# Performance work log

Hardware: AMD Instinct MI355X
Metric: run time of the kernel (lower is better)

## Reference

```python
import jax, jax.numpy as jnp
import numpy as np

VOCAB, EMB, HID, OUT = 50257, 256, 512, 2

def setup_inputs() -> dict:
    key = jax.random.key(0)
    ks = jax.random.split(key, 8)
    s_e = 1.0  # nn.Embedding default N(0,1)
    emb = jax.random.normal(ks[0], (VOCAB, EMB), dtype=jnp.float32) * s_e
    emb = emb.at[0].set(0.0)  # padding_idx=0
    def lin(k1, k2, fan_in, fan_out):
        bound = 1.0 / np.sqrt(fan_in)
        w = jax.random.uniform(k1, (fan_out, fan_in), minval=-bound, maxval=bound, dtype=jnp.float32)
        b = jax.random.uniform(k2, (fan_out,), minval=-bound, maxval=bound, dtype=jnp.float32)
        return w, b
    Ww, Wb = lin(ks[1], ks[2], EMB, HID)
    Uw, Ub = lin(ks[3], ks[4], HID, HID)
    Vw, Vb = lin(ks[5], ks[6], HID, OUT)
    x = jax.random.randint(ks[7], (128, 512), 0, VOCAB, dtype=jnp.int64)
    return {"x": x, "emb": emb, "Ww": Ww, "Wb": Wb, "Uw": Uw, "Ub": Ub, "Vw": Vw, "Vb": Vb}

def reference(x, emb, Ww, Wb, Uw, Ub, Vw, Vb):
    # x: [B, T] int tokens -> embed: [B, T, E]
    xe = emb[x]
    # Precompute input projections for all timesteps in one big GEMM: [B, T, H]
    wx = jnp.einsum('bte,he->bth', xe, Ww) + Wb
    B = x.shape[0]
    h0 = jnp.zeros((B, Uw.shape[0]), dtype=xe.dtype)
    def step(h, wx_t):
        h_new = jnp.tanh(wx_t + h @ Uw.T + Ub)
        return h_new, None
    hT, _ = jax.lax.scan(step, h0, jnp.swapaxes(wx, 0, 1))  # scan over time [T, B, H]
    logits = hT @ Vw.T + Vb  # [B, OUT]
    return logits
```

## Files before the change

kernel.cpp:

```cpp
#include <hip/hip_runtime.h>
#include <hip/hip_bf16.h>
#include <math.h>


#define VOCAB   50257
#define T_STEPS 512
#define HID     512
#define EMB     256

typedef __bf16 bf16x8 __attribute__((ext_vector_type(8)));
typedef float  f32x4  __attribute__((ext_vector_type(4)));
typedef float  f32x2  __attribute__((ext_vector_type(2)));
typedef int    i32x4  __attribute__((ext_vector_type(4)));

__device__ inline float ldf(const void* p, long i, bool f32) {
    if (f32) return ((const float*)p)[i];
    unsigned bits = ((unsigned)((const unsigned short*)p)[i]) << 16;
    return __uint_as_float(bits);
}
__device__ inline void stf(void* p, long i, float v, bool f32) {
    if (f32) { ((float*)p)[i] = v; return; }
    unsigned b = __float_as_uint(v);
    unsigned r = (b + 0x7fffu + ((b >> 16) & 1u)) >> 16;
    ((unsigned short*)p)[i] = (unsigned short)r;
}
__device__ inline unsigned short f2bf(float v) {
    unsigned b = __float_as_uint(v);
    return (unsigned short)((b + 0x7fffu + ((b >> 16) & 1u)) >> 16);
}
__device__ inline float bf2f(unsigned short u) {
    return __uint_as_float(((unsigned)u) << 16);
}
__device__ inline int get_tok(const int* x, int idx, bool x64) {
    unsigned u = (unsigned)(x64 ? x[2 * idx] : x[idx]);
    return (u < (unsigned)VOCAB) ? (int)u : 0;
}
__device__ inline int detect_flags(const int* x, const void* emb) {
    int allz = 1;
    const unsigned short* e16 = (const unsigned short*)emb;
    for (int i = 256; i < 320; ++i) allz &= (e16[i] == 0);
    int x64 = 1;
    for (int j = 1; j < 16; j += 2) x64 &= (x[j] == 0);
    return allz | (x64 << 1);
}
__device__ inline float tanh_f(float x) {
    float ax = fabsf(x);
    float e  = __expf(-2.0f * ax);
    float t  = (1.0f - e) * __builtin_amdgcn_rcpf(1.0f + e);
    return copysignf(t, x);
}
__device__ inline unsigned tq(float v) {
    float x = fminf(3.5f, fmaxf(-3.5f, v));
    float s = x * x;
    float num = x * fmaf(s, fmaf(s, 127.0f, 13335.0f), 120015.0f);
    float den = fmaf(s, fmaf(s, 15.0f, 420.0f), 945.0f);
    float f = fmaf(num, __builtin_amdgcn_rcpf(den), 12582912.0f);
    return __float_as_uint(f) & 0xffu;
}
__device__ inline unsigned tq2(float a, float b) {
    f32x2 x;
    x.x = fminf(3.5f, fmaxf(-3.5f, a));
    x.y = fminf(3.5f, fmaxf(-3.5f, b));
    f32x2 s   = x * x;
    f32x2 num = x * (s * (s * 127.0f + 13335.0f) + 120015.0f);
    f32x2 den = s * (s * 15.0f + 420.0f) + 945.0f;
    float f0 = fmaf(num.x, __builtin_amdgcn_rcpf(den.x), 12582912.0f);
    float f1 = fmaf(num.y, __builtin_amdgcn_rcpf(den.y), 12582912.0f);
    return (__float_as_uint(f0) & 0xffu) | ((__float_as_uint(f1) & 0xffu) << 8);
}

#define XEPAD 264
__global__ __launch_bounds__(1024) void wx_gemm(
    const int* __restrict__ x, const void* __restrict__ embv,
    const void* __restrict__ Wwv, const void* __restrict__ Wbv,
    const void* __restrict__ Ubv, unsigned char* __restrict__ ws)
{
    __shared__ __align__(16) __hip_bfloat16 xe_s[64][XEPAD];
    __shared__ int flags_s;
    const int t = blockIdx.x, tid = threadIdx.x;
    if (tid == 0) flags_s = detect_flags(x, embv);
    __syncthreads();
    const bool f32w = (flags_s & 1) != 0;
    const bool x64  = (flags_s & 2) != 0;

    const int w = tid >> 6, lane = tid & 63, ln = lane & 15, q = lane >> 4;

    bf16x8 bf[2][8];
    float  bias[2];
#pragma unroll
    for (int tn = 0; tn < 2; ++tn) {
        long n = w * 32 + tn * 16 + ln;
        bias[tn] = ldf(Wbv, n, f32w) + ldf(Ubv, n, f32w);
#pragma unroll
        for (int kt = 0; kt < 8; ++kt) {
            bf16x8 v;
#pragma unroll
            for (int j = 0; j < 8; ++j)
                v[j] = (__bf16)ldf(Wwv, n * EMB + kt * 32 + q * 8 + j, f32w);
            bf[tn][kt] = v;
        }
    }

    for (int half = 0; half < 2; ++half) {
        {
            int row = tid >> 4, sub = tid & 15;
            int tok = get_tok(x, (half * 64 + row) * T_STEPS + t, x64);
#pragma unroll
            for (int i = 0; i < 4; ++i) {
                int col = sub * 4 + i * 64;
                float v0, v1, v2, v3;
                if (f32w) {
                    const float4 vv = *(const float4*)((const float*)embv
                                        + (long)tok * EMB + col);
                    v0 = vv.x; v1 = vv.y; v2 = vv.z; v3 = vv.w;
                } else {
                    const unsigned short* e = (const unsigned short*)embv
                                        + (long)tok * EMB + col;
                    v0 = bf2f(e[0]); v1 = bf2f(e[1]);
                    v2 = bf2f(e[2]); v3 = bf2f(e[3]);
                }
                __hip_bfloat16* d = &xe_s[row][col];
                d[0] = __float2bfloat16(v0); d[1] = __float2bfloat16(v1);
                d[2] = __float2bfloat16(v2); d[3] = __float2bfloat16(v3);
            }
        }
        __syncthreads();

#pragma unroll
        for (int bt = 0; bt < 4; ++bt) {
            f32x4 acc[2];
#pragma unroll
            for (int tn = 0; tn < 2; ++tn)
#pragma unroll
                for (int r = 0; r < 4; ++r) acc[tn][r] = bias[tn];
#pragma unroll
            for (int kt = 0; kt < 8; ++kt) {
                bf16x8 a = *(const bf16x8*)&xe_s[bt * 16 + ln][kt * 32 + q * 8];
#pragma unroll
                for (int tn = 0; tn < 2; ++tn)
                    acc[tn] = __builtin_amdgcn_mfma_f32_16x16x32_bf16(
                        a, bf[tn][kt], acc[tn], 0, 0, 0);
            }
            {
                int g = half * 4 + bt;
                unsigned short o8[8];
#pragma unroll
                for (int tn = 0; tn < 2; ++tn)
#pragma unroll
                    for (int r = 0; r < 4; ++r)
                        o8[tn * 4 + r] = f2bf(acc[tn][r]);
                long ofs = (((long)t * 8 + g) * 1024 + tid) * 16;
                *(uint4*)(ws + ofs) = *(const uint4*)o8;
            }
        }
        __syncthreads();
    }
}

#define HQP 528
__global__ __launch_bounds__(1024) void scan_i8(
    const void* __restrict__ Uwv, const void* __restrict__ Vwv,
    const void* __restrict__ Vbv, const int* __restrict__ x,
    const void* __restrict__ embv, const unsigned char* __restrict__ wsc,
    void* __restrict__ outv)
{
    __shared__ __align__(16) signed char hq[2][16][HQP];
    __shared__ float red[1024];
    __shared__ int flags_s;

    const int tid = threadIdx.x, g = blockIdx.x, b0 = g * 16;
    if (tid == 0) flags_s = detect_flags(x, embv);
    __syncthreads();
    const bool f32w = (flags_s & 1) != 0;

    const int w = tid >> 6, lane = tid & 63, ln = lane & 15, q = lane >> 4;

    {
        float mx = 0.0f;
        if (f32w) {
            const float4* U4 = (const float4*)Uwv;
            for (int i = tid; i < 65536; i += 1024) {
                float4 v = U4[i];
                mx = fmaxf(mx, fmaxf(fmaxf(fabsf(v.x), fabsf(v.y)),
                                     fmaxf(fabsf(v.z), fabsf(v.w))));
            }
        } else {
            for (long i = tid; i < 262144; i += 1024)
                mx = fmaxf(mx, fabsf(ldf(Uwv, i, false)));
        }
        red[tid] = mx;
        __syncthreads();
        for (int s = 512; s > 0; s >>= 1) {
            if (tid < s) red[tid] = fmaxf(red[tid], red[tid + s]);
            __syncthreads();
        }
    }
    const float su = red[0];
    const float qs = 127.0f / su;
    const float sc = su / 16129.0f;

    i32x4 uq[2][8];
#pragma unroll
    for (int tn = 0; tn < 2; ++tn) {
        long n = w * 32 + tn * 16 + ln;
#pragma unroll
        for (int kt = 0; kt < 8; ++kt) {
            i32x4 frag;
#pragma unroll
            for (int wd = 0; wd < 4; ++wd) {
                unsigned pk = 0;
#pragma unroll
                for (int jb = 0; jb < 4; ++jb) {
                    int kp = kt * 64 + q * 16 + wd * 4 + jb;
                    int kl = (kp & ~31) | ((kp & 1) << 4) | ((kp >> 1) & 15);
                    float v = ldf(Uwv, n * HID + kl, f32w) * qs;
                    int   qv = (int)__builtin_rintf(v);
                    qv = qv > 127 ? 127 : (qv < -127 ? -127 : qv);
                    pk |= ((unsigned)(unsigned char)(signed char)qv) << (8 * jb);
                }
                frag[wd] = (int)pk;
            }
            uq[tn][kt] = frag;
        }
    }

    for (int i = tid; i < 16 * HQP; i += 1024) ((signed char*)hq[0])[i] = 0;
    __syncthreads();

    const unsigned char* wxp = wsc + ((long)g * 1024 + tid) * 16;
    const long wx_step = 8L * 1024 * 16;

    uint4 wv = *(const uint4*)wxp;
    const unsigned char* wp = wxp + wx_step;

    for (int t = 0; t < T_STEPS; ++t) {
        uint4 wvn = *(const uint4*)((t + 1 < T_STEPS) ? wp : wxp);
        wp += wx_step;

        i32x4 acc0 = {0, 0, 0, 0}, acc1 = {0, 0, 0, 0};
        const signed char (*hr)[HQP] = hq[t & 1];
#pragma unroll
        for (int ktb = 0; ktb < 2; ++ktb) {
            i32x4 afr[4];
#pragma unroll
            for (int k = 0; k < 4; ++k)
                afr[k] = *(const i32x4*)&hr[ln][(ktb * 4 + k) * 64 + q * 16];
#pragma unroll
            for (int k = 0; k < 4; ++k) {
                acc0 = __builtin_amdgcn_mfma_i32_16x16x64_i8(
                    afr[k], uq[0][ktb * 4 + k], acc0, 0, 0, 0);
                acc1 = __builtin_amdgcn_mfma_i32_16x16x64_i8(
                    afr[k], uq[1][ktb * 4 + k], acc1, 0, 0, 0);
            }
        }

        float wx0[4], wx1[4];
        wx0[0] = __uint_as_float(wv.x << 16); wx0[1] = __uint_as_float(wv.x & 0xffff0000u);
        wx0[2] = __uint_as_float(wv.y << 16); wx0[3] = __uint_as_float(wv.y & 0xffff0000u);
        wx1[0] = __uint_as_float(wv.z << 16); wx1[1] = __uint_as_float(wv.z & 0xffff0000u);
        wx1[2] = __uint_as_float(wv.w << 16); wx1[3] = __uint_as_float(wv.w & 0xffff0000u);

        signed char (*hw)[HQP] = hq[(t + 1) & 1];
#pragma unroll
        for (int r = 0; r < 4; ++r) {
            unsigned c01 = tq2(fmaf((float)acc0[r], sc, wx0[r]),
                               fmaf((float)acc1[r], sc, wx1[r]));
            *(unsigned short*)&hw[q * 4 + r][w * 32 + ln * 2] =
                (unsigned short)c01;
        }
        asm volatile("s_waitcnt lgkmcnt(0)" ::: "memory");
        __builtin_amdgcn_s_barrier();
        wv = wvn;
    }

    if (tid < 512) {
        int b = tid >> 5, o = (tid >> 4) & 1, kp = tid & 15;
        float s = 0.0f;
#pragma unroll 4
        for (int j = 0; j < 32; ++j) {
            int kph = kp * 32 + j;
            int kl = (kph & ~31) | ((kph & 1) << 4) | ((kph >> 1) & 15);
            s += (float)hq[0][b][kph] * (1.0f / 127.0f)
               * ldf(Vwv, (long)o * HID + kl, f32w);
        }
        s += __shfl_xor(s, 1);
        s += __shfl_xor(s, 2);
        s += __shfl_xor(s, 4);
        s += __shfl_xor(s, 8);
        if (kp == 0)
            stf(outv, (long)(b0 + b) * 2 + o, s + ldf(Vbv, o, f32w), f32w);
    }
}

#define XPAD 264
#define HPAD 528
#define BPG  4
#define R7_WS_H   4096
#define R7_WS_NEED (4096 + 2 * 8 * 16 * 256 * 4)

__device__ inline void load_xe(const void* emb, long base, bool f32,
                               bf16x8* a, bf16x8* b) {
    if (f32) {
        const float* p = (const float*)emb + base;
        bf16x8 va, vb;
#pragma unroll
        for (int j = 0; j < 8; ++j) va[j] = (__bf16)p[j];
#pragma unroll
        for (int j = 0; j < 8; ++j) vb[j] = (__bf16)p[8 + j];
        *a = va; *b = vb;
    } else {
        const bf16x8* p = (const bf16x8*)((const unsigned short*)emb + base);
        *a = p[0]; *b = p[1];
    }
}

__global__ __launch_bounds__(256, 1) void scan_mfma_fb(
    const int* __restrict__ x, const void* __restrict__ embv,
    const void* __restrict__ Wwv, const void* __restrict__ Wbv,
    const void* __restrict__ Uwv, const void* __restrict__ Ubv,
    const void* __restrict__ Vwv, const void* __restrict__ Vbv,
    unsigned char* __restrict__ ws, void* __restrict__ outv)
{
    __shared__ __align__(16) __hip_bfloat16 xe_s[16][XPAD];
    __shared__ __align__(16) __hip_bfloat16 hbuf[2][16][HPAD];
    __shared__ int flags_s;

    const int tid = threadIdx.x;
    const int g   = blockIdx.x >> 2;
    const int cg  = blockIdx.x & 3;
    const int b0  = g * 16;

    if (tid == 0) flags_s = detect_flags(x, embv);
    __syncthreads();
    const bool f32w = (flags_s & 1) != 0;
    const bool x64  = (flags_s & 2) != 0;

    const int w = tid >> 6, lane = tid & 63, ln = lane & 15, q = lane >> 4;
    const int n0 = cg * 128 + w * 32 + ln;

    for (int i = tid; i < 2 * 16 * HPAD; i += 256)
        ((__hip_bfloat16*)hbuf)[i] = __float2bfloat16(0.0f);

    bf16x8 ufr[2][16], wfr[2][8];
#pragma unroll
    for (int half = 0; half < 2; ++half) {
        const long n = n0 + half * 16;
#pragma unroll
        for (int kt = 0; kt < 16; ++kt) {
            bf16x8 v;
#pragma unroll
            for (int j = 0; j < 8; ++j)
                v[j] = (__bf16)ldf(Uwv, n * HID + kt * 32 + q * 8 + j, f32w);
            ufr[half][kt] = v;
        }
#pragma unroll
        for (int kt = 0; kt < 8; ++kt) {
            bf16x8 v;
#pragma unroll
            for (int j = 0; j < 8; ++j)
                v[j] = (__bf16)ldf(Wwv, n * EMB + kt * 32 + q * 8 + j, f32w);
            wfr[half][kt] = v;
        }
    }
    const float bias0 = ldf(Wbv, n0, f32w)      + ldf(Ubv, n0, f32w);
    const float bias1 = ldf(Wbv, n0 + 16, f32w) + ldf(Ubv, n0 + 16, f32w);

    const int xr = tid >> 4, xc = (tid & 15) * 16;
    {
        int tok = get_tok(x, (b0 + xr) * T_STEPS + 0, x64);
        bf16x8 xa, xb;
        load_xe(embv, (long)tok * EMB + xc, f32w, &xa, &xb);
        *(bf16x8*)&xe_s[xr][xc]     = xa;
        *(bf16x8*)&xe_s[xr][xc + 8] = xb;
    }
    __syncthreads();

    unsigned*           hg32 = (unsigned*)(ws + R7_WS_H);
    unsigned long long* hg64 = (unsigned long long*)(ws + R7_WS_H);
    int*                cnt  = (int*)(void*)ws + g * 32;

    for (int t = 0; t < T_STEPS; ++t) {
        bf16x8 nxa, nxb;
        const bool have_next = (t + 1 < T_STEPS);
        if (have_next) {
            int tok = get_tok(x, (b0 + xr) * T_STEPS + (t + 1), x64);
            load_xe(embv, (long)tok * EMB + xc, f32w, &nxa, &nxb);
        }

        f32x4 acc0, acc1;
#pragma unroll
        for (int r = 0; r < 4; ++r) { acc0[r] = bias0; acc1[r] = bias1; }
#pragma unroll
        for (int kt = 0; kt < 8; ++kt) {
            bf16x8 a = *(const bf16x8*)&xe_s[ln][kt * 32 + q * 8];
            acc0 = __builtin_amdgcn_mfma_f32_16x16x32_bf16(a, wfr[0][kt], acc0, 0, 0, 0);
            acc1 = __builtin_amdgcn_mfma_f32_16x16x32_bf16(a, wfr[1][kt], acc1, 0, 0, 0);
        }
        const __hip_bfloat16 (*hr)[HPAD] = hbuf[t & 1];
#pragma unroll
        for (int kt = 0; kt < 16; ++kt) {
            bf16x8 a = *(const bf16x8*)&hr[ln][kt * 32 + q * 8];
            acc0 = __builtin_amdgcn_mfma_f32_16x16x32_bf16(a, ufr[0][kt], acc0, 0, 0, 0);
            acc1 = __builtin_amdgcn_mfma_f32_16x16x32_bf16(a, ufr[1][kt], acc1, 0, 0, 0);
        }

        const int nb = (t + 1) & 1;
        {
            unsigned* dst = hg32 + (size_t)(nb * 8 + g) * 4096 + cg * 64 + w * 16 + ln;
#pragma unroll
            for (int r = 0; r < 4; ++r) {
                unsigned word = (unsigned)f2bf(tanh_f(acc0[r]))
                              | ((unsigned)f2bf(tanh_f(acc1[r])) << 16);
                __hip_atomic_store(dst + (size_t)(q * 4 + r) * 256, word,
                                   __ATOMIC_RELAXED, __HIP_MEMORY_SCOPE_AGENT);
            }
        }
        asm volatile("s_waitcnt vmcnt(0)" ::: "memory");
        __syncthreads();

        if (have_next) {
            *(bf16x8*)&xe_s[xr][xc]     = nxa;
            *(bf16x8*)&xe_s[xr][xc + 8] = nxb;
        }

        if (tid == 0) {
            __hip_atomic_fetch_add(cnt, 1, __ATOMIC_RELAXED,
                                   __HIP_MEMORY_SCOPE_AGENT);
            const int target = BPG * (t + 1);
            while (__hip_atomic_load(cnt, __ATOMIC_RELAXED,
                                     __HIP_MEMORY_SCOPE_AGENT) < target)
                __builtin_amdgcn_s_sleep(1);
        }
        __syncthreads();

        {
            const unsigned long long* src = hg64 + (size_t)(nb * 8 + g) * 2048;
#pragma unroll
            for (int m = tid; m < 2048; m += 256) {
                unsigned long long v = __hip_atomic_load(
                    src + m, __ATOMIC_RELAXED, __HIP_MEMORY_SCOPE_AGENT);
                int row = m >> 7, p = m & 127;
                int j0  = 2 * p;
                int cgp = j0 >> 6, wv = (j0 >> 4) & 3, l0 = j0 & 15;
                int colA = cgp * 128 + wv * 32 + l0;
                unsigned w0 = (unsigned)v, w1 = (unsigned)(v >> 32);
                unsigned lo = (w0 & 0xffffu) | (w1 << 16);
                unsigned hi = (w0 >> 16) | (w1 & 0xffff0000u);
                *(unsigned*)&hbuf[nb][row][colA]      = lo;
                *(unsigned*)&hbuf[nb][row][colA + 16] = hi;
            }
        }
        __syncthreads();
    }

    if (cg == 0) {
        int b = tid >> 4, rem = tid & 15, o = rem >> 3, kp = rem & 7;
        float s = 0.0f;
#pragma unroll 4
        for (int j = 0; j < 64; ++j) {
            int k = kp * 64 + j;
            s += __bfloat162float(hbuf[0][b][k]) * ldf(Vwv, (long)o * HID + k, f32w);
        }
        s += __shfl_xor(s, 1);
        s += __shfl_xor(s, 2);
        s += __shfl_xor(s, 4);
        if (kp == 0)
            stf(outv, (long)(b0 + b) * 2 + o, s + ldf(Vbv, o, f32w), f32w);
    }
}

#define B_PER 2
__global__ __launch_bounds__(512) void fixup(
    const int* __restrict__ x, const void* __restrict__ emb,
    const void* __restrict__ Ww, const void* __restrict__ Wb,
    const void* __restrict__ Uw, const void* __restrict__ Ub,
    const void* __restrict__ Vw, const void* __restrict__ Vb,
    void* __restrict__ out, int force)
{
    __shared__ float h_s[2][B_PER][HID];
    __shared__ float xe_sf[B_PER][EMB];
    __shared__ int   flags_s, bad_s;

    const int tid = threadIdx.x;
    const int b0  = blockIdx.x * B_PER;

    if (tid == 0) {
        int fl = detect_flags(x, emb);
        flags_s = fl;
        int bad = force;
        if (!force) {
            bool f32o = (fl & 1) != 0;
            for (int i = 0; i < 2 * B_PER; ++i) {
                int oi = b0 * 2 + i;
                if (f32o) {
                    float v = ((const float*)out)[oi];
                    bad |= (v != v);
                } else {
                    unsigned short u = ((const unsigned short*)out)[oi];
                    bad |= (((u & 0x7F80u) == 0x7F80u) && ((u & 0x7Fu) != 0));
                }
            }
        }
        bad_s = bad;
    }
    __syncthreads();
    if (!bad_s) return;

    const bool f32w = (flags_s & 1) != 0;
    const bool x64  = (flags_s & 2) != 0;
    const int n = tid;
    const float bias = ldf(Wb, n, f32w) + ldf(Ub, n, f32w);

    for (int b = 0; b < B_PER; ++b) h_s[0][b][n] = 0.0f;

    for (int t = 0; t < T_STEPS; ++t) {
        {
            int b = tid >> 8, c = tid & 255;
            int tok = get_tok(x, (b0 + b) * T_STEPS + t, x64);
            xe_sf[b][c] = ldf(emb, (long)tok * EMB + c, f32w);
        }
        __syncthreads();

        float acc0 = bias, acc1 = bias;
        const long wrow = (long)n * EMB;
#pragma unroll 8
        for (int k = 0; k < EMB; ++k) {
            float wv = ldf(Ww, wrow + k, f32w);
            acc0 += xe_sf[0][k] * wv;
            acc1 += xe_sf[1][k] * wv;
        }
        const long urow = (long)n * HID;
        const float* hc0 = h_s[t & 1][0];
        const float* hc1 = h_s[t & 1][1];
#pragma unroll 8
        for (int k = 0; k < HID; ++k) {
            float uv = ldf(Uw, urow + k, f32w);
            acc0 += hc0[k] * uv;
            acc1 += hc1[k] * uv;
        }
        h_s[(t + 1) & 1][0][n] = tanhf(acc0);
        h_s[(t + 1) & 1][1][n] = tanhf(acc1);
        __syncthreads();
    }

    if (tid < 2 * B_PER) {
        int b = tid >> 1, o = tid & 1;
        float s = ldf(Vb, o, f32w);
        for (int k = 0; k < HID; ++k)
            s += h_s[0][b][k] * ldf(Vw, (long)o * HID + k, f32w);
        stf(out, (b0 + b) * 2 + o, s, f32w);
    }
}

extern "C" void kernel_launch(void* const* d_in, const int* in_sizes, int n_in,
                              void* d_out, int out_size, void* d_ws, size_t ws_size,
                              hipStream_t stream) {
    const int* x = (const int*)d_in[0];
    const size_t WX16 = (size_t)T_STEPS * 128 * 512 * 2;
    if (ws_size >= WX16) {
        wx_gemm<<<512, 1024, 0, stream>>>(
            x, d_in[1], d_in[2], d_in[3], d_in[5], (unsigned char*)d_ws);
        scan_i8<<<8, 1024, 0, stream>>>(
            d_in[4], d_in[6], d_in[7], x, d_in[1],
            (const unsigned char*)d_ws, d_out);
        fixup<<<64, 512, 0, stream>>>(
            x, d_in[1], d_in[2], d_in[3], d_in[4], d_in[5], d_in[6], d_in[7],
            d_out, 0);
    } else if (ws_size >= (size_t)R7_WS_NEED) {
        hipMemsetAsync(d_ws, 0, 4096, stream);
        scan_mfma_fb<<<32, 256, 0, stream>>>(
            x, d_in[1], d_in[2], d_in[3], d_in[4], d_in[5], d_in[6], d_in[7],
            (unsigned char*)d_ws, d_out);
        fixup<<<64, 512, 0, stream>>>(
            x, d_in[1], d_in[2], d_in[3], d_in[4], d_in[5], d_in[6], d_in[7],
            d_out, 0);
    } else {
        fixup<<<64, 512, 0, stream>>>(
            x, d_in[1], d_in[2], d_in[3], d_in[4], d_in[5], d_in[6], d_in[7],
            d_out, 1);
    }
}
```

Measured before the change: 946.7 us.

## Halve scan block to 8 waves with 64 hidden columns per wave

The int8 MFMA recurrent scan now runs with 512 threads per block instead of 1024. Each wave owns 64 output columns (four MFMA tiles) rather than 32, so it keeps twice as many quantized U fragments in registers. The hidden-state column permutation and the wx load addressing are remapped to match. The goal is a cheaper per-step barrier across fewer waves and more reuse of each A fragment, at the cost of higher register pressure and less wave-level parallelism per step.

Result: slower. 1.039 ms (+9.8%).

```diff
diff --git a/kernel.cpp b/kernel.cpp
--- a/kernel.cpp
+++ b/kernel.cpp
@@ -158,14 +158,14 @@
 }
 
 #define HQP 528
-__global__ __launch_bounds__(1024) void scan_i8(
+__global__ __launch_bounds__(512, 2) void scan_i8(
     const void* __restrict__ Uwv, const void* __restrict__ Vwv,
     const void* __restrict__ Vbv, const int* __restrict__ x,
     const void* __restrict__ embv, const unsigned char* __restrict__ wsc,
     void* __restrict__ outv)
 {
     __shared__ __align__(16) signed char hq[2][16][HQP];
-    __shared__ float red[1024];
+    __shared__ float red[512];
     __shared__ int flags_s;
 
     const int tid = threadIdx.x, g = blockIdx.x, b0 = g * 16;
@@ -179,18 +179,18 @@
         float mx = 0.0f;
         if (f32w) {
             const float4* U4 = (const float4*)Uwv;
-            for (int i = tid; i < 65536; i += 1024) {
+            for (int i = tid; i < 65536; i += 512) {
                 float4 v = U4[i];
                 mx = fmaxf(mx, fmaxf(fmaxf(fabsf(v.x), fabsf(v.y)),
                                      fmaxf(fabsf(v.z), fabsf(v.w))));
             }
         } else {
-            for (long i = tid; i < 262144; i += 1024)
+            for (long i = tid; i < 262144; i += 512)
                 mx = fmaxf(mx, fabsf(ldf(Uwv, i, false)));
         }
         red[tid] = mx;
         __syncthreads();
-        for (int s = 512; s > 0; s >>= 1) {
+        for (int s = 256; s > 0; s >>= 1) {
             if (tid < s) red[tid] = fmaxf(red[tid], red[tid + s]);
             __syncthreads();
         }
@@ -199,10 +199,10 @@
     const float qs = 127.0f / su;
     const float sc = su / 16129.0f;
 
-    i32x4 uq[2][8];
-#pragma unroll
-    for (int tn = 0; tn < 2; ++tn) {
-        long n = w * 32 + tn * 16 + ln;
+    i32x4 uq[4][8];
+#pragma unroll
+    for (int tn = 0; tn < 4; ++tn) {
+        long n = w * 64 + tn * 16 + ln;
 #pragma unroll
         for (int kt = 0; kt < 8; ++kt) {
             i32x4 frag;
@@ -212,7 +212,7 @@
 #pragma unroll
                 for (int jb = 0; jb < 4; ++jb) {
                     int kp = kt * 64 + q * 16 + wd * 4 + jb;
-                    int kl = (kp & ~31) | ((kp & 1) << 4) | ((kp >> 1) & 15);
+                    int kl = (kp & ~63) | ((kp & 3) << 4) | ((kp >> 2) & 15);
                     float v = ldf(Uwv, n * HID + kl, f32w) * qs;
                     int   qv = (int)__builtin_rintf(v);
                     qv = qv > 127 ? 127 : (qv < -127 ? -127 : qv);
@@ -224,20 +224,28 @@
         }
     }
 
-    for (int i = tid; i < 16 * HQP; i += 1024) ((signed char*)hq[0])[i] = 0;
+    for (int i = tid; i < 16 * HQP; i += 512) ((signed char*)hq[0])[i] = 0;
     __syncthreads();
 
-    const unsigned char* wxp = wsc + ((long)g * 1024 + tid) * 16;
+    const unsigned char* wxp = wsc + ((long)g * 1024 + (w * 128 + q * 16 + ln)) * 16;
     const long wx_step = 8L * 1024 * 16;
 
-    uint4 wv = *(const uint4*)wxp;
+    uint4 wa = *(const uint4*)wxp;
+    uint4 wb = *(const uint4*)(wxp + 1024);
     const unsigned char* wp = wxp + wx_step;
 
     for (int t = 0; t < T_STEPS; ++t) {
-        uint4 wvn = *(const uint4*)((t + 1 < T_STEPS) ? wp : wxp);
+        const unsigned char* pp = (t + 1 < T_STEPS) ? wp : wxp;
+        uint4 wan = *(const uint4*)pp;
+        uint4 wbn = *(const uint4*)(pp + 1024);
         wp += wx_step;
 
-        i32x4 acc0 = {0, 0, 0, 0}, acc1 = {0, 0, 0, 0};
+        i32x4 acc[4];
+#pragma unroll
+        for (int tn = 0; tn < 4; ++tn)
+#pragma unroll
+            for (int r = 0; r < 4; ++r) acc[tn][r] = 0;
+
         const signed char (*hr)[HQP] = hq[t & 1];
 #pragma unroll
         for (int ktb = 0; ktb < 2; ++ktb) {
@@ -246,40 +254,44 @@
             for (int k = 0; k < 4; ++k)
                 afr[k] = *(const i32x4*)&hr[ln][(ktb * 4 + k) * 64 + q * 16];
 #pragma unroll
-            for (int k = 0; k < 4; ++k) {
-                acc0 = __builtin_amdgcn_mfma_i32_16x16x64_i8(
-                    afr[k], uq[0][ktb * 4 + k], acc0, 0, 0, 0);
-                acc1 = __builtin_amdgcn_mfma_i32_16x16x64_i8(
-                    afr[k], uq[1][ktb * 4 + k], acc1, 0, 0, 0);
-            }
-        }
-
-        float wx0[4], wx1[4];
-        wx0[0] = __uint_as_float(wv.x << 16); wx0[1] = __uint_as_float(wv.x & 0xffff0000u);
-        wx0[2] = __uint_as_float(wv.y << 16); wx0[3] = __uint_as_float(wv.y & 0xffff0000u);
-        wx1[0] = __uint_as_float(wv.z << 16); wx1[1] = __uint_as_float(wv.z & 0xffff0000u);
-        wx1[2] = __uint_as_float(wv.w << 16); wx1[3] = __uint_as_float(wv.w & 0xffff0000u);
+            for (int k = 0; k < 4; ++k)
+#pragma unroll
+                for (int tn = 0; tn < 4; ++tn)
+                    acc[tn] = __builtin_amdgcn_mfma_i32_16x16x64_i8(
+                        afr[k], uq[tn][ktb * 4 + k], acc[tn], 0, 0, 0);
+        }
+
+        float wx0[4], wx1[4], wx2[4], wx3[4];
+        wx0[0] = __uint_as_float(wa.x << 16); wx0[1] = __uint_as_float(wa.x & 0xffff0000u);
+        wx0[2] = __uint_as_float(wa.y << 16); wx0[3] = __uint_as_float(wa.y & 0xffff0000u);
+        wx1[0] = __uint_as_float(wa.z << 16); wx1[1] = __uint_as_float(wa.z & 0xffff0000u);
+        wx1[2] = __uint_as_float(wa.w << 16); wx1[3] = __uint_as_float(wa.w & 0xffff0000u);
+        wx2[0] = __uint_as_float(wb.x << 16); wx2[1] = __uint_as_float(wb.x & 0xffff0000u);
+        wx2[2] = __uint_as_float(wb.y << 16); wx2[3] = __uint_as_float(wb.y & 0xffff0000u);
+        wx3[0] = __uint_as_float(wb.z << 16); wx3[1] = __uint_as_float(wb.z & 0xffff0000u);
+        wx3[2] = __uint_as_float(wb.w << 16); wx3[3] = __uint_as_float(wb.w & 0xffff0000u);
 
         signed char (*hw)[HQP] = hq[(t + 1) & 1];
 #pragma unroll
         for (int r = 0; r < 4; ++r) {
-            unsigned c01 = tq2(fmaf((float)acc0[r], sc, wx0[r]),
-                               fmaf((float)acc1[r], sc, wx1[r]));
-            *(unsigned short*)&hw[q * 4 + r][w * 32 + ln * 2] =
-                (unsigned short)c01;
+            unsigned lo = tq2(fmaf((float)acc[0][r], sc, wx0[r]),
+                              fmaf((float)acc[1][r], sc, wx1[r]));
+            unsigned hi = tq2(fmaf((float)acc[2][r], sc, wx2[r]),
+                              fmaf((float)acc[3][r], sc, wx3[r]));
+            *(unsigned*)&hw[q * 4 + r][w * 64 + ln * 4] = lo | (hi << 16);
         }
         asm volatile("s_waitcnt lgkmcnt(0)" ::: "memory");
         __builtin_amdgcn_s_barrier();
-        wv = wvn;
-    }
-
-    if (tid < 512) {
+        wa = wan; wb = wbn;
+    }
+
+    {
         int b = tid >> 5, o = (tid >> 4) & 1, kp = tid & 15;
         float s = 0.0f;
 #pragma unroll 4
         for (int j = 0; j < 32; ++j) {
             int kph = kp * 32 + j;
-            int kl = (kph & ~31) | ((kph & 1) << 4) | ((kph >> 1) & 15);
+            int kl = (kph & ~63) | ((kph & 3) << 4) | ((kph >> 2) & 15);
             s += (float)hq[0][b][kph] * (1.0f / 127.0f)
                * ldf(Vwv, (long)o * HID + kl, f32w);
         }
@@ -560,7 +572,7 @@
     if (ws_size >= WX16) {
         wx_gemm<<<512, 1024, 0, stream>>>(
             x, d_in[1], d_in[2], d_in[3], d_in[5], (unsigned char*)d_ws);
-        scan_i8<<<8, 1024, 0, stream>>>(
+        scan_i8<<<8, 512, 0, stream>>>(
             d_in[4], d_in[6], d_in[7], x, d_in[1],
             (const unsigned char*)d_ws, d_out);
         fixup<<<64, 512, 0, stream>>>(
```
